# Performance work log

Hardware: AMD Instinct MI355X
Metric: run time of the kernel (lower is better)

Reference implementation:

```python
import jax, jax.numpy as jnp
import numpy as np

N_NODES = 100000
N_EDGES = 1600000
IN_DIM = 64
HID_DIM = 64
OUT_DIM = 1


def setup_inputs() -> dict:
    key = jax.random.key(0)
    ks = jax.random.split(key, 5)
    x = jax.random.normal(ks[0], (N_NODES, IN_DIM), dtype=jnp.float32)
    edge_index = jax.random.randint(ks[1], (2, N_EDGES), 0, N_NODES, dtype=jnp.int64)
    s1 = 1.0 / np.sqrt(IN_DIM)
    s2 = 1.0 / np.sqrt(HID_DIM)
    W1 = jax.random.normal(ks[2], (IN_DIM, HID_DIM), dtype=jnp.float32) * s1
    b1 = jnp.zeros((HID_DIM,), dtype=jnp.float32)
    W2 = jax.random.normal(ks[3], (HID_DIM, HID_DIM), dtype=jnp.float32) * s2
    b2 = jnp.zeros((HID_DIM,), dtype=jnp.float32)
    Wp = jax.random.normal(ks[4], (HID_DIM, OUT_DIM), dtype=jnp.float32) * s2
    bp = jnp.zeros((OUT_DIM,), dtype=jnp.float32)
    return {"x": x, "edge_index": edge_index, "W1": W1, "b1": b1,
            "W2": W2, "b2": b2, "Wp": Wp, "bp": bp}


def _gcn_conv(x, src, dst, deg_inv_sqrt, W, b):
    # PyG GCNConv: linear transform, then deg-normalized scatter-add aggregation
    h = x @ W  # [N, out]
    norm = deg_inv_sqrt[src] * deg_inv_sqrt[dst]  # [E_total]
    msg = h[src] * norm[:, None]  # gather + scale, [E_total, out]
    agg = jax.ops.segment_sum(msg, dst, num_segments=x.shape[0])
    return agg + b


def reference(x, edge_index, W1, b1, W2, b2, Wp, bp):
    n = x.shape[0]
    # add self-loops (as PyG GCNConv does by default)
    loop = jnp.arange(n, dtype=edge_index.dtype)
    src = jnp.concatenate([edge_index[0], loop])
    dst = jnp.concatenate([edge_index[1], loop])
    # symmetric normalization from in-degree over dst (includes self-loops)
    deg = jax.ops.segment_sum(jnp.ones_like(dst, dtype=x.dtype), dst, num_segments=n)
    deg_inv_sqrt = jnp.where(deg > 0, jax.lax.rsqrt(jnp.maximum(deg, 1e-12)), 0.0)
    h = jax.nn.relu(_gcn_conv(x, src, dst, deg_inv_sqrt, W1, b1))
    # dropout(p=0.3) is identity at eval time
    h = jax.nn.relu(_gcn_conv(h, src, dst, deg_inv_sqrt, W2, b2))
    return h @ Wp + bp  # [N, OUT_DIM]
```

## Files before the change

kernel.cpp:

```cpp
#include <hip/hip_runtime.h>
#include <hip/hip_fp16.h>


#define GNN_N 100000
#define GNN_E 1600000
#define NBUCK 391
#define NBLK  256
#define EPB   6250
#define SCTILE 16

__global__ __launch_bounds__(256) void k_hist(const int* __restrict__ dst,
                                              int* __restrict__ hist) {
    __shared__ int h[NBUCK];
    for (int i = threadIdx.x; i < NBUCK; i += 256) h[i] = 0;
    __syncthreads();
    int b = blockIdx.x;
    int e0 = b * EPB, e1 = min(e0 + EPB, GNN_E);
    for (int e = e0 + threadIdx.x; e < e1; e += 256)
        atomicAdd(&h[dst[e] >> 8], 1);
    __syncthreads();
    for (int i = threadIdx.x; i < NBUCK; i += 256)
        hist[b * NBUCK + i] = h[i];
}

__global__ __launch_bounds__(256) void k_cscan(int* __restrict__ hist,
                                               int* __restrict__ tot) {
    __shared__ int tile[256][SCTILE + 1];
    int k0 = blockIdx.x * SCTILE;
    int b = threadIdx.x;
#pragma unroll
    for (int i = 0; i < SCTILE; ++i) {
        int k = k0 + i;
        tile[b][i] = (k < NBUCK) ? hist[b * NBUCK + k] : 0;
    }
    __syncthreads();
    int lane = b & 63, w = b >> 6;
    int cSub = lane >> 4;
    int l16 = lane & 15;
    int col = w * 4 + cSub;
    int run = 0;
    for (int chunk = 0; chunk < 16; ++chunk) {
        int idx = chunk * 16 + l16;
        int v = tile[idx][col];
        int s = v;
#pragma unroll
        for (int o = 1; o < 16; o <<= 1) {
            int t = __shfl_up(s, o);
            if (l16 >= o) s += t;
        }
        tile[idx][col] = s - v + run;
        run += __shfl(s, lane | 15);
    }
    if (l16 == 0 && k0 + col < NBUCK) tot[k0 + col] = run;
    __syncthreads();
#pragma unroll
    for (int i = 0; i < SCTILE; ++i) {
        int k = k0 + i;
        if (k < NBUCK) hist[b * NBUCK + k] = tile[b][i];
    }
}

__global__ __launch_bounds__(512) void k_btot(const int* __restrict__ tot,
                                              int* __restrict__ bbase) {
    __shared__ int s[NBUCK];
    int t = threadIdx.x;
    if (t < NBUCK) s[t] = tot[t];
    __syncthreads();
    if (t == 0) {
        int run = 0;
        for (int i = 0; i < NBUCK; ++i) { int v = s[i]; s[i] = run; run += v; }
    }
    __syncthreads();
    if (t < NBUCK) bbase[t] = s[t];
    if (t == 0) bbase[NBUCK] = GNN_E;
}

__global__ __launch_bounds__(256) void k_part(const int* __restrict__ src,
                                              const int* __restrict__ dst,
                                              const int* __restrict__ hist,
                                              const int* __restrict__ bbase,
                                              unsigned int* __restrict__ part) {
    __shared__ int off[NBUCK];
    int b = blockIdx.x;
    for (int i = threadIdx.x; i < NBUCK; i += 256)
        off[i] = bbase[i] + hist[b * NBUCK + i];
    __syncthreads();
    int e0 = b * EPB, e1 = min(e0 + EPB, GNN_E);
    for (int e = e0 + threadIdx.x; e < e1; e += 256) {
        int d = dst[e], s = src[e];
        int slot = atomicAdd(&off[d >> 8], 1);
        part[slot] = ((unsigned int)(d & 255) << 17) | (unsigned int)s;
    }
}

__global__ __launch_bounds__(256) void k_bsort(const unsigned int* __restrict__ part,
                                               const int* __restrict__ bbase,
                                               int* __restrict__ csr,
                                               int* __restrict__ rowptr,
                                               int* __restrict__ deg,
                                               float* __restrict__ dis) {
    __shared__ int cnt[256];
    __shared__ int pos[256];
    int k = blockIdx.x;
    int t = threadIdx.x;
    cnt[t] = 0;
    __syncthreads();
    int e0 = bbase[k], e1 = bbase[k + 1];
    for (int e = e0 + t; e < e1; e += 256)
        atomicAdd(&cnt[part[e] >> 17], 1);
    __syncthreads();
    if (t == 0) {
        int run = 0;
        for (int i = 0; i < 256; ++i) { int c = cnt[i]; pos[i] = run; run += c; }
    }
    __syncthreads();
    int node = k * 256 + t;
    if (node < GNN_N) {
        rowptr[node] = e0 + pos[t];
        deg[node]    = cnt[t];
        dis[node]    = rsqrtf((float)cnt[t] + 1.0f);
    }
    __syncthreads();
    for (int e = e0 + t; e < e1; e += 256) {
        unsigned int p = part[e];
        int slot = e0 + atomicAdd(&pos[p >> 17], 1);
        csr[slot] = (int)(p & 0x1FFFF) << 7;
    }
}

template<typename TIN>
__global__ __launch_bounds__(256) void k_mm64h(const TIN* __restrict__ X,
                                               const float* __restrict__ W,
                                               const float* __restrict__ dis,
                                               __half* __restrict__ Y, int n) {
    __shared__ float  Xs[64][68];
    __shared__ float4 Wsh[64 * 16];
    int tid = threadIdx.x;
    int base = blockIdx.x * 64;
    for (int i = tid; i < 1024; i += 256)
        Wsh[i] = ((const float4*)W)[i];
    if constexpr (sizeof(TIN) == 4) {
#pragma unroll
        for (int i = 0; i < 4; ++i) {
            int g = i * 256 + tid;
            int r = g >> 4, c4 = g & 15;
            int row = base + r;
            float4 v = (row < n) ? ((const float4*)(X + (size_t)row * 64))[c4]
                                 : make_float4(0.f, 0.f, 0.f, 0.f);
            *(float4*)&Xs[r][c4 * 4] = v;
        }
    } else {
#pragma unroll
        for (int i = 0; i < 2; ++i) {
            int g = i * 256 + tid;
            int r = g >> 3, c8 = g & 7;
            int row = base + r;
            float f[8];
            if (row < n) {
                uint4 u = *(const uint4*)((const __half*)X + (size_t)row * 64 + c8 * 8);
                float2 t0 = __half22float2(*(__half2*)&u.x);
                float2 t1 = __half22float2(*(__half2*)&u.y);
                float2 t2 = __half22float2(*(__half2*)&u.z);
                float2 t3 = __half22float2(*(__half2*)&u.w);
                f[0] = t0.x; f[1] = t0.y; f[2] = t1.x; f[3] = t1.y;
                f[4] = t2.x; f[5] = t2.y; f[6] = t3.x; f[7] = t3.y;
            } else {
#pragma unroll
                for (int z = 0; z < 8; ++z) f[z] = 0.f;
            }
            *(float4*)&Xs[r][c8 * 8 + 0] = make_float4(f[0], f[1], f[2], f[3]);
            *(float4*)&Xs[r][c8 * 8 + 4] = make_float4(f[4], f[5], f[6], f[7]);
        }
    }
    __syncthreads();
    int tj = tid & 15;
    int ti = tid >> 4;
    float4 a0 = {0,0,0,0}, a1 = {0,0,0,0}, a2 = {0,0,0,0}, a3 = {0,0,0,0};
#pragma unroll 1
    for (int k4 = 0; k4 < 16; ++k4) {
        float4 x0 = *(const float4*)&Xs[ti * 4 + 0][k4 * 4];
        float4 x1 = *(const float4*)&Xs[ti * 4 + 1][k4 * 4];
        float4 x2 = *(const float4*)&Xs[ti * 4 + 2][k4 * 4];
        float4 x3 = *(const float4*)&Xs[ti * 4 + 3][k4 * 4];
        float4 w0 = Wsh[(k4 * 4 + 0) * 16 + tj];
        float4 w1 = Wsh[(k4 * 4 + 1) * 16 + tj];
        float4 w2 = Wsh[(k4 * 4 + 2) * 16 + tj];
        float4 w3 = Wsh[(k4 * 4 + 3) * 16 + tj];
#define FMA4(A, XV)                                                      \
        A.x += XV.x * w0.x + XV.y * w1.x + XV.z * w2.x + XV.w * w3.x;    \
        A.y += XV.x * w0.y + XV.y * w1.y + XV.z * w2.y + XV.w * w3.y;    \
        A.z += XV.x * w0.z + XV.y * w1.z + XV.z * w2.z + XV.w * w3.z;    \
        A.w += XV.x * w0.w + XV.y * w1.w + XV.z * w2.w + XV.w * w3.w;
        FMA4(a0, x0) FMA4(a1, x1) FMA4(a2, x2) FMA4(a3, x3)
#undef FMA4
    }
#pragma unroll
    for (int q = 0; q < 4; ++q) {
        int row = base + ti * 4 + q;
        if (row < n) {
            float d = dis[row];
            float4 a = (q == 0) ? a0 : (q == 1) ? a1 : (q == 2) ? a2 : a3;
            __half2 p0 = __floats2half2_rn(a.x * d, a.y * d);
            __half2 p1 = __floats2half2_rn(a.z * d, a.w * d);
            __half2* yp = (__half2*)(Y + (size_t)row * 64);
            yp[tj * 2 + 0] = p0;
            yp[tj * 2 + 1] = p1;
        }
    }
}

#define ACC8(A, U) {                                                     \
    float2 f_;                                                           \
    f_ = __half22float2(*(__half2*)&U.x); A[0] += f_.x; A[1] += f_.y;    \
    f_ = __half22float2(*(__half2*)&U.y); A[2] += f_.x; A[3] += f_.y;    \
    f_ = __half22float2(*(__half2*)&U.z); A[4] += f_.x; A[5] += f_.y;    \
    f_ = __half22float2(*(__half2*)&U.w); A[6] += f_.x; A[7] += f_.y; }

template<bool HEAD>
__global__ __launch_bounds__(256) void k_gatherg(
        const __half* __restrict__ T, const int* __restrict__ csr,
        const int* __restrict__ rowptr, const int* __restrict__ deg,
        const float* __restrict__ dis, const float* __restrict__ bias,
        const float* __restrict__ Wp, const float* __restrict__ bp,
        void* __restrict__ outv, int n) {
    int tid = threadIdx.x;
    int q = tid & 7;
    int node = blockIdx.x * 32 + (tid >> 3);
    if (node >= n) return;
    int base = rowptr[node];
    int cnt  = deg[node];
    float dd = dis[node];
    const char* Tq = (const char*)T + q * 16;
    float a0[8], a1[8];
#pragma unroll
    for (int i = 0; i < 8; ++i) { a0[i] = 0.f; a1[i] = 0.f; }
    int j = 0;
    for (; j + 4 <= cnt; j += 4) {
        int s0 = csr[base + j + 0];
        int s1 = csr[base + j + 1];
        int s2 = csr[base + j + 2];
        int s3 = csr[base + j + 3];
        uint4 u0 = *(const uint4*)(Tq + (size_t)(unsigned)s0);
        uint4 u1 = *(const uint4*)(Tq + (size_t)(unsigned)s1);
        uint4 u2 = *(const uint4*)(Tq + (size_t)(unsigned)s2);
        uint4 u3 = *(const uint4*)(Tq + (size_t)(unsigned)s3);
        ACC8(a0, u0)
        ACC8(a1, u1)
        ACC8(a0, u2)
        ACC8(a1, u3)
    }
    if (j + 2 <= cnt) {
        int s0 = csr[base + j + 0];
        int s1 = csr[base + j + 1];
        uint4 u0 = *(const uint4*)(Tq + (size_t)(unsigned)s0);
        uint4 u1 = *(const uint4*)(Tq + (size_t)(unsigned)s1);
        ACC8(a0, u0)
        ACC8(a1, u1)
        j += 2;
    }
    if (j < cnt) {
        int s = csr[base + j];
        uint4 u = *(const uint4*)(Tq + (size_t)(unsigned)s);
        ACC8(a0, u)
    }
    uint4 us = *(const uint4*)(Tq + (size_t)node * 128);
    ACC8(a1, us)
    float4 bb0 = ((const float4*)bias)[q * 2 + 0];
    float4 bb1 = ((const float4*)bias)[q * 2 + 1];
    float r[8];
    r[0] = fmaxf(dd * (a0[0] + a1[0]) + bb0.x, 0.f);
    r[1] = fmaxf(dd * (a0[1] + a1[1]) + bb0.y, 0.f);
    r[2] = fmaxf(dd * (a0[2] + a1[2]) + bb0.z, 0.f);
    r[3] = fmaxf(dd * (a0[3] + a1[3]) + bb0.w, 0.f);
    r[4] = fmaxf(dd * (a0[4] + a1[4]) + bb1.x, 0.f);
    r[5] = fmaxf(dd * (a0[5] + a1[5]) + bb1.y, 0.f);
    r[6] = fmaxf(dd * (a0[6] + a1[6]) + bb1.z, 0.f);
    r[7] = fmaxf(dd * (a0[7] + a1[7]) + bb1.w, 0.f);
    if constexpr (HEAD) {
        float4 w0 = ((const float4*)Wp)[q * 2 + 0];
        float4 w1 = ((const float4*)Wp)[q * 2 + 1];
        float s = r[0] * w0.x + r[1] * w0.y + r[2] * w0.z + r[3] * w0.w
                + r[4] * w1.x + r[5] * w1.y + r[6] * w1.z + r[7] * w1.w;
#pragma unroll
        for (int m = 1; m <= 4; m <<= 1) s += __shfl_xor(s, m);
        if (q == 0) ((float*)outv)[node] = s + bp[0];
    } else {
        __half* op = (__half*)outv + (size_t)node * 64 + q * 8;
        __half2 h0 = __floats2half2_rn(r[0], r[1]);
        __half2 h1 = __floats2half2_rn(r[2], r[3]);
        __half2 h2 = __floats2half2_rn(r[4], r[5]);
        __half2 h3 = __floats2half2_rn(r[6], r[7]);
        uint4 u;
        *(__half2*)&u.x = h0; *(__half2*)&u.y = h1;
        *(__half2*)&u.z = h2; *(__half2*)&u.w = h3;
        *(uint4*)op = u;
    }
}

extern "C" void kernel_launch(void* const* d_in, const int* in_sizes, int n_in,
                              void* d_out, int out_size, void* d_ws, size_t ws_size,
                              hipStream_t stream) {
    const float* x  = (const float*)d_in[0];
    const int*   ei = (const int*)d_in[1];
    const float* W1 = (const float*)d_in[2];
    const float* b1 = (const float*)d_in[3];
    const float* W2 = (const float*)d_in[4];
    const float* b2 = (const float*)d_in[5];
    const float* Wp = (const float*)d_in[6];
    const float* bp = (const float*)d_in[7];
    float* out = (float*)d_out;

    const int N = GNN_N, E = GNN_E;
    const int* srcv = ei;
    const int* dstv = ei + E;

    char* ws = (char*)d_ws;
    int*    hist   = (int*)(ws + 0);
    int*    bbase  = (int*)(ws + 400896);
    int*    rowptr = (int*)(ws + 402944);
    int*    deg    = (int*)(ws + 802944);
    float*  dis    = (float*)(ws + 1202944);
    int*    tot    = (int*)(ws + 1202944);
    int*    csr    = (int*)(ws + 1603584);
    __half* TA     = (__half*)(ws + 8003584);
    __half* h1h    = (__half*)(ws + 20803584);
    __half* TB     = (__half*)(ws + 33603584);
    unsigned int* part = (unsigned int*)(ws + 46403584);

    k_hist <<<NBLK, 256, 0, stream>>>(dstv, hist);
    k_cscan<<<(NBUCK + SCTILE - 1) / SCTILE, 256, 0, stream>>>(hist, tot);
    k_btot <<<1, 512, 0, stream>>>(tot, bbase);
    k_part <<<NBLK, 256, 0, stream>>>(srcv, dstv, hist, bbase, part);
    k_bsort<<<NBUCK, 256, 0, stream>>>(part, bbase, csr, rowptr, deg, dis);

    k_mm64h<float><<<(N + 63) / 64, 256, 0, stream>>>(x, W1, dis, TA, N);
    k_gatherg<false><<<(N + 31) / 32, 256, 0, stream>>>(TA, csr, rowptr, deg, dis,
                                                        b1, nullptr, nullptr, h1h, N);
    k_mm64h<__half><<<(N + 63) / 64, 256, 0, stream>>>(h1h, W2, dis, TB, N);
    k_gatherg<true><<<(N + 31) / 32, 256, 0, stream>>>(TB, csr, rowptr, deg, dis,
                                                       b2, Wp, bp, out, N);
}
```

Measured before the change: 152.7 us.

## Pad CSR rows to multiples of four with dummy zero row, vectorize index loads

Each node's CSR row is padded to a multiple of 4 entries. The padding points at a zeroed dummy row placed past the end of TA and TB, so the gather kernel can read neighbour indices as int4 and unroll by 8 without scalar tails. The histogram and partition kernels now read dst and src as int4, with the block count changed to 250 of 6400 edges each so the int4 loads stay aligned. The bucket sort stages its partition in LDS to avoid a second global read. In exchange the CSR buffer is larger, the padded slots add extra gathers, and the workspace layout is changed.

```diff
diff --git a/kernel.cpp b/kernel.cpp
--- a/kernel.cpp
+++ b/kernel.cpp
@@ -5,19 +5,34 @@
 #define GNN_N 100000
 #define GNN_E 1600000
 #define NBUCK 391
-#define NBLK  256
-#define EPB   6250
+#define NBLK  250
+#define EPB   6400
 #define SCTILE 16
+#define STAGE_CAP 4864
+#define DUMMY_OFF (GNN_N * 128)
 
 __global__ __launch_bounds__(256) void k_hist(const int* __restrict__ dst,
-                                              int* __restrict__ hist) {
+                                              int* __restrict__ hist,
+                                              __half* __restrict__ TA,
+                                              __half* __restrict__ TB) {
     __shared__ int h[NBUCK];
     for (int i = threadIdx.x; i < NBUCK; i += 256) h[i] = 0;
+    if (blockIdx.x == 0 && threadIdx.x < 16) {
+        uint4 z = {0, 0, 0, 0};
+        int t = threadIdx.x;
+        __half* base = (t < 8) ? TA : TB;
+        *(uint4*)((char*)base + DUMMY_OFF + (t & 7) * 16) = z;
+    }
     __syncthreads();
     int b = blockIdx.x;
     int e0 = b * EPB, e1 = min(e0 + EPB, GNN_E);
-    for (int e = e0 + threadIdx.x; e < e1; e += 256)
-        atomicAdd(&h[dst[e] >> 8], 1);
+    for (int e = e0 + threadIdx.x * 4; e < e1; e += 1024) {
+        int4 d = *(const int4*)(dst + e);
+        atomicAdd(&h[d.x >> 8], 1);
+        atomicAdd(&h[d.y >> 8], 1);
+        atomicAdd(&h[d.z >> 8], 1);
+        atomicAdd(&h[d.w >> 8], 1);
+    }
     __syncthreads();
     for (int i = threadIdx.x; i < NBUCK; i += 256)
         hist[b * NBUCK + i] = h[i];
@@ -31,7 +46,7 @@
 #pragma unroll
     for (int i = 0; i < SCTILE; ++i) {
         int k = k0 + i;
-        tile[b][i] = (k < NBUCK) ? hist[b * NBUCK + k] : 0;
+        tile[b][i] = (k < NBUCK && b < NBLK) ? hist[b * NBUCK + k] : 0;
     }
     __syncthreads();
     int lane = b & 63, w = b >> 6;
@@ -56,12 +71,13 @@
 #pragma unroll
     for (int i = 0; i < SCTILE; ++i) {
         int k = k0 + i;
-        if (k < NBUCK) hist[b * NBUCK + k] = tile[b][i];
+        if (k < NBUCK && b < NBLK) hist[b * NBUCK + k] = tile[b][i];
     }
 }
 
 __global__ __launch_bounds__(512) void k_btot(const int* __restrict__ tot,
-                                              int* __restrict__ bbase) {
+                                              int* __restrict__ bbase,
+                                              int* __restrict__ cbase) {
     __shared__ int s[NBUCK];
     int t = threadIdx.x;
     if (t < NBUCK) s[t] = tot[t];
@@ -71,7 +87,10 @@
         for (int i = 0; i < NBUCK; ++i) { int v = s[i]; s[i] = run; run += v; }
     }
     __syncthreads();
-    if (t < NBUCK) bbase[t] = s[t];
+    if (t < NBUCK) {
+        bbase[t] = s[t];
+        cbase[t] = (s[t] & ~3) + t * 772;
+    }
     if (t == 0) bbase[NBUCK] = GNN_E;
 }
 
@@ -86,45 +105,72 @@
         off[i] = bbase[i] + hist[b * NBUCK + i];
     __syncthreads();
     int e0 = b * EPB, e1 = min(e0 + EPB, GNN_E);
-    for (int e = e0 + threadIdx.x; e < e1; e += 256) {
-        int d = dst[e], s = src[e];
-        int slot = atomicAdd(&off[d >> 8], 1);
-        part[slot] = ((unsigned int)(d & 255) << 17) | (unsigned int)s;
+    for (int e = e0 + threadIdx.x * 4; e < e1; e += 1024) {
+        int4 d = *(const int4*)(dst + e);
+        int4 s = *(const int4*)(src + e);
+        int sl0 = atomicAdd(&off[d.x >> 8], 1);
+        part[sl0] = ((unsigned int)(d.x & 255) << 17) | (unsigned int)s.x;
+        int sl1 = atomicAdd(&off[d.y >> 8], 1);
+        part[sl1] = ((unsigned int)(d.y & 255) << 17) | (unsigned int)s.y;
+        int sl2 = atomicAdd(&off[d.z >> 8], 1);
+        part[sl2] = ((unsigned int)(d.z & 255) << 17) | (unsigned int)s.z;
+        int sl3 = atomicAdd(&off[d.w >> 8], 1);
+        part[sl3] = ((unsigned int)(d.w & 255) << 17) | (unsigned int)s.w;
     }
 }
 
 __global__ __launch_bounds__(256) void k_bsort(const unsigned int* __restrict__ part,
                                                const int* __restrict__ bbase,
+                                               const int* __restrict__ cbase,
                                                int* __restrict__ csr,
                                                int* __restrict__ rowptr,
                                                int* __restrict__ deg,
                                                float* __restrict__ dis) {
     __shared__ int cnt[256];
-    __shared__ int pos[256];
+    __shared__ int pstart[256];
+    __shared__ int bump[256];
+    __shared__ unsigned int stage[STAGE_CAP];
     int k = blockIdx.x;
     int t = threadIdx.x;
     cnt[t] = 0;
     __syncthreads();
     int e0 = bbase[k], e1 = bbase[k + 1];
-    for (int e = e0 + t; e < e1; e += 256)
-        atomicAdd(&cnt[part[e] >> 17], 1);
+    int m = e1 - e0;
+    bool fits = (m <= STAGE_CAP);
+    for (int i = t; i < m; i += 256) {
+        unsigned int p = part[e0 + i];
+        if (fits) stage[i] = p;
+        atomicAdd(&cnt[p >> 17], 1);
+    }
     __syncthreads();
     if (t == 0) {
         int run = 0;
-        for (int i = 0; i < 256; ++i) { int c = cnt[i]; pos[i] = run; run += c; }
-    }
-    __syncthreads();
+        for (int i = 0; i < 256; ++i) {
+            pstart[i] = run;
+            run += (cnt[i] + 3) & ~3;
+        }
+    }
+    __syncthreads();
+    int cb = cbase[k];
     int node = k * 256 + t;
     if (node < GNN_N) {
-        rowptr[node] = e0 + pos[t];
-        deg[node]    = cnt[t];
-        dis[node]    = rsqrtf((float)cnt[t] + 1.0f);
-    }
-    __syncthreads();
-    for (int e = e0 + t; e < e1; e += 256) {
-        unsigned int p = part[e];
-        int slot = e0 + atomicAdd(&pos[p >> 17], 1);
-        csr[slot] = (int)(p & 0x1FFFF) << 7;
+        int c = cnt[t];
+        rowptr[node] = cb + pstart[t];
+        deg[node]    = (c + 3) & ~3;
+        dis[node]    = rsqrtf((float)c + 1.0f);
+    }
+    bump[t] = pstart[t];
+    __syncthreads();
+    for (int i = t; i < m; i += 256) {
+        unsigned int p = fits ? stage[i] : part[e0 + i];
+        int slot = atomicAdd(&bump[p >> 17], 1);
+        csr[cb + slot] = (int)(p & 0x1FFFF) << 7;
+    }
+    __syncthreads();
+    if (node < GNN_N) {
+        int c = cnt[t], pc = (c + 3) & ~3;
+        for (int i = c; i < pc; ++i)
+            csr[cb + pstart[t] + i] = DUMMY_OFF;
     }
 }
 
@@ -235,33 +281,27 @@
 #pragma unroll
     for (int i = 0; i < 8; ++i) { a0[i] = 0.f; a1[i] = 0.f; }
     int j = 0;
-    for (; j + 4 <= cnt; j += 4) {
-        int s0 = csr[base + j + 0];
-        int s1 = csr[base + j + 1];
-        int s2 = csr[base + j + 2];
-        int s3 = csr[base + j + 3];
-        uint4 u0 = *(const uint4*)(Tq + (size_t)(unsigned)s0);
-        uint4 u1 = *(const uint4*)(Tq + (size_t)(unsigned)s1);
-        uint4 u2 = *(const uint4*)(Tq + (size_t)(unsigned)s2);
-        uint4 u3 = *(const uint4*)(Tq + (size_t)(unsigned)s3);
-        ACC8(a0, u0)
-        ACC8(a1, u1)
-        ACC8(a0, u2)
-        ACC8(a1, u3)
-    }
-    if (j + 2 <= cnt) {
-        int s0 = csr[base + j + 0];
-        int s1 = csr[base + j + 1];
-        uint4 u0 = *(const uint4*)(Tq + (size_t)(unsigned)s0);
-        uint4 u1 = *(const uint4*)(Tq + (size_t)(unsigned)s1);
-        ACC8(a0, u0)
-        ACC8(a1, u1)
-        j += 2;
+    for (; j + 8 <= cnt; j += 8) {
+        int4 c0 = *(const int4*)(csr + base + j);
+        int4 c1 = *(const int4*)(csr + base + j + 4);
+        uint4 u0 = *(const uint4*)(Tq + (size_t)(unsigned)c0.x);
+        uint4 u1 = *(const uint4*)(Tq + (size_t)(unsigned)c0.y);
+        uint4 u2 = *(const uint4*)(Tq + (size_t)(unsigned)c0.z);
+        uint4 u3 = *(const uint4*)(Tq + (size_t)(unsigned)c0.w);
+        uint4 u4 = *(const uint4*)(Tq + (size_t)(unsigned)c1.x);
+        uint4 u5 = *(const uint4*)(Tq + (size_t)(unsigned)c1.y);
+        uint4 u6 = *(const uint4*)(Tq + (size_t)(unsigned)c1.z);
+        uint4 u7 = *(const uint4*)(Tq + (size_t)(unsigned)c1.w);
+        ACC8(a0, u0) ACC8(a1, u1) ACC8(a0, u2) ACC8(a1, u3)
+        ACC8(a0, u4) ACC8(a1, u5) ACC8(a0, u6) ACC8(a1, u7)
     }
     if (j < cnt) {
-        int s = csr[base + j];
-        uint4 u = *(const uint4*)(Tq + (size_t)(unsigned)s);
-        ACC8(a0, u)
+        int4 c0 = *(const int4*)(csr + base + j);
+        uint4 u0 = *(const uint4*)(Tq + (size_t)(unsigned)c0.x);
+        uint4 u1 = *(const uint4*)(Tq + (size_t)(unsigned)c0.y);
+        uint4 u2 = *(const uint4*)(Tq + (size_t)(unsigned)c0.z);
+        uint4 u3 = *(const uint4*)(Tq + (size_t)(unsigned)c0.w);
+        ACC8(a0, u0) ACC8(a1, u1) ACC8(a0, u2) ACC8(a1, u3)
     }
     uint4 us = *(const uint4*)(Tq + (size_t)node * 128);
     ACC8(a1, us)
@@ -316,22 +356,23 @@
 
     char* ws = (char*)d_ws;
     int*    hist   = (int*)(ws + 0);
-    int*    bbase  = (int*)(ws + 400896);
-    int*    rowptr = (int*)(ws + 402944);
-    int*    deg    = (int*)(ws + 802944);
-    float*  dis    = (float*)(ws + 1202944);
-    int*    tot    = (int*)(ws + 1202944);
-    int*    csr    = (int*)(ws + 1603584);
-    __half* TA     = (__half*)(ws + 8003584);
-    __half* h1h    = (__half*)(ws + 20803584);
-    __half* TB     = (__half*)(ws + 33603584);
-    unsigned int* part = (unsigned int*)(ws + 46403584);
-
-    k_hist <<<NBLK, 256, 0, stream>>>(dstv, hist);
+    int*    bbase  = (int*)(ws + 392000);
+    int*    cbase  = (int*)(ws + 393600);
+    int*    rowptr = (int*)(ws + 395264);
+    int*    deg    = (int*)(ws + 795264);
+    float*  dis    = (float*)(ws + 1195264);
+    int*    tot    = (int*)(ws + 1195264);
+    int*    csr    = (int*)(ws + 1595392);
+    __half* TA     = (__half*)(ws + 9600000);
+    __half* h1h    = (__half*)(ws + 22400256);
+    __half* TB     = (__half*)(ws + 35200384);
+    unsigned int* part = (unsigned int*)(ws + 48000512);
+
+    k_hist <<<NBLK, 256, 0, stream>>>(dstv, hist, TA, TB);
     k_cscan<<<(NBUCK + SCTILE - 1) / SCTILE, 256, 0, stream>>>(hist, tot);
-    k_btot <<<1, 512, 0, stream>>>(tot, bbase);
+    k_btot <<<1, 512, 0, stream>>>(tot, bbase, cbase);
     k_part <<<NBLK, 256, 0, stream>>>(srcv, dstv, hist, bbase, part);
-    k_bsort<<<NBUCK, 256, 0, stream>>>(part, bbase, csr, rowptr, deg, dis);
+    k_bsort<<<NBUCK, 256, 0, stream>>>(part, bbase, cbase, csr, rowptr, deg, dis);
 
     k_mm64h<float><<<(N + 63) / 64, 256, 0, stream>>>(x, W1, dis, TA, N);
     k_gatherg<false><<<(N + 31) / 32, 256, 0, stream>>>(TA, csr, rowptr, deg, dis,
```

Result: faster. 147.7 us (-3.3%).
